# Optimization experiments

Measured on AMD Instinct MI355X. Metric: run time of the kernel, lower is better.

The kernel has to match this reference:

```python
import jax, jax.numpy as jnp
import numpy as np

ALPHA, BETA, GAMMA = 1.0, 0.01, 0.1
COS_EPS = 1e-8  # torch F.cosine_similarity eps


def setup_inputs() -> dict:
    key = jax.random.key(0)
    k1, k2, k3, k4 = jax.random.split(key, 4)
    B, C = 4096, 1000
    N, D = 8192, 256
    return {
        "pred": jax.random.normal(k1, (B, C), dtype=jnp.float32),
        "target": jax.random.randint(k2, (B,), 0, C, dtype=jnp.int64),
        "adj_matrix": jax.random.uniform(k3, (N, N), dtype=jnp.float32),
        "node_embeddings": jax.random.normal(k4, (N, D), dtype=jnp.float32),
    }


def reference(pred, target, adj_matrix, node_embeddings):
    # L_task: mean cross-entropy over logits
    logp = jax.nn.log_softmax(pred, axis=-1)                      # [B, C]
    l_task = -jnp.mean(jnp.take_along_axis(logp, target[:, None], axis=1))

    # L_sparse: mean |adj|
    l_sparse = jnp.mean(jnp.abs(adj_matrix))

    # L_semantic: cosine similarity via normalize + matmul (avoids NxNxD intermediate)
    norms = jnp.linalg.norm(node_embeddings, axis=1)              # [N]
    dots = node_embeddings @ node_embeddings.T                    # [N, N]
    sim = dots / jnp.maximum(norms[:, None] * norms[None, :], COS_EPS)
    l_semantic = jnp.mean(adj_matrix * (1.0 - sim))

    return ALPHA * l_task + BETA * l_sparse + GAMMA * l_semantic
```

## Files before the change

### kernel.cpp

```cpp
#include <hip/hip_runtime.h>
#include <hip/hip_bf16.h>
#include <stdint.h>
#include <stddef.h>

#define N_NODES 8192
#define DIM     256
#define BATCH   4096
#define CLASSES 1000
#define ALPHA_C 1.0f
#define BETA_C  0.01f
#define GAMMA_C 0.1f

#define KSPLIT  16
#define KRANGE  (N_NODES / KSPLIT)
#define NCHUNK  (KRANGE / 64)
#define BM      64

typedef __bf16 bf16_t;
typedef __bf16 bf16x8 __attribute__((ext_vector_type(8)));
typedef float  f32x4  __attribute__((ext_vector_type(4)));
typedef float  f32x16 __attribute__((ext_vector_type(16)));

__device__ __forceinline__ void async16(const void* g, void* l) {
  __builtin_amdgcn_global_load_lds(
      (const __attribute__((address_space(1))) uint32_t*)g,
      (__attribute__((address_space(3))) uint32_t*)l, 16, 0, 0);
}

__global__ __launch_bounds__(256) void prep_norm(
    const float* __restrict__ emb, bf16_t* __restrict__ U) {
  const int row = blockIdx.x;
  const int t = threadIdx.x;
  const float v = emb[(size_t)row * DIM + t];
  float sq = v * v;
  for (int off = 32; off; off >>= 1) sq += __shfl_down(sq, off);
  __shared__ float red[4];
  if ((t & 63) == 0) red[t >> 6] = sq;
  __syncthreads();
  const float total = red[0] + red[1] + red[2] + red[3];
  U[(size_t)row * DIM + t] = (bf16_t)(v * rsqrtf(total));
}

#define TP 68

__global__ __launch_bounds__(256) void prep_transpose(
    const bf16_t* __restrict__ U, bf16_t* __restrict__ V) {
  __shared__ bf16_t tile[64 * TP];
  const int k0 = blockIdx.x * 64;
  const int d0 = blockIdx.y * 64;
  const int t = threadIdx.x;
  const int r = t >> 3;
  const int c8 = t & 7;

  *(bf16x8*)&tile[r * TP + c8 * 8] =
      *(const bf16x8*)&U[(size_t)(k0 + r) * DIM + d0 + c8 * 8];
  *(bf16x8*)&tile[(r + 32) * TP + c8 * 8] =
      *(const bf16x8*)&U[(size_t)(k0 + r + 32) * DIM + d0 + c8 * 8];
  __syncthreads();

  bf16x8 o0, o1;
#pragma unroll
  for (int j = 0; j < 8; ++j) {
    o0[j] = tile[(c8 * 8 + j) * TP + r];
    o1[j] = tile[(c8 * 8 + j) * TP + r + 32];
  }
  *(bf16x8*)&V[(size_t)(d0 + r) * N_NODES + k0 + c8 * 8] = o0;
  *(bf16x8*)&V[(size_t)(d0 + r + 32) * N_NODES + k0 + c8 * 8] = o1;
}

__global__ __launch_bounds__(256) void ce_kernel(
    const float* __restrict__ pred, const int* __restrict__ target,
    float* __restrict__ out) {
  const int row = blockIdx.x;
  const int t = threadIdx.x;
  const float* p = pred + (size_t)row * CLASSES;

  float v[4];
  for (int k = 0; k < 4; ++k) {
    const int c = t + k * 256;
    v[k] = (c < CLASSES) ? p[c] : -INFINITY;
  }

  float m = fmaxf(fmaxf(v[0], v[1]), fmaxf(v[2], v[3]));
  for (int off = 32; off; off >>= 1) m = fmaxf(m, __shfl_down(m, off));

  __shared__ float red[8];
  const int wave = t >> 6, lane = t & 63;
  if (lane == 0) red[wave] = m;
  __syncthreads();
  if (t == 0) red[4] = fmaxf(fmaxf(red[0], red[1]), fmaxf(red[2], red[3]));
  __syncthreads();
  const float mx = red[4];

  float s = 0.f;
  for (int k = 0; k < 4; ++k) s += __expf(v[k] - mx);
  for (int off = 32; off; off >>= 1) s += __shfl_down(s, off);
  if (lane == 0) red[wave] = s;
  __syncthreads();
  if (t == 0) {
    float ssum = red[0] + red[1] + red[2] + red[3];
    float lse = mx + __logf(ssum);
    float loss = lse - p[target[row]];
    atomicAdd(out, loss * (ALPHA_C / (float)BATCH));
  }
}

__global__ __launch_bounds__(256) void gemm_kernel(
    const float* __restrict__ adj, const bf16_t* __restrict__ U,
    const bf16_t* __restrict__ V, float* __restrict__ out) {
  __shared__ __align__(16) bf16_t As[BM * 64];
  __shared__ __align__(16) bf16_t Bs[DIM * 64];

  const int i0 = blockIdx.x * BM;
  const int kbase = blockIdx.y * KRANGE;
  const int t = threadIdx.x;
  const int w = t >> 6, lane = t & 63;
  const int m = lane & 31, h = lane >> 5;

  const int ar = t >> 3;
  const int ac = t & 7;
  const int srow = lane >> 3;
  const int sch = (lane & 7) ^ srow;

  f32x16 acc[2][2] = {};
  float sa = 0.f, sabs = 0.f;

  float4 pf[4];
  {
    const float* a0p = adj + (size_t)(i0 + ar) * N_NODES + kbase + ac * 8;
    const float* a1p = adj + (size_t)(i0 + ar + 32) * N_NODES + kbase + ac * 8;
    pf[0] = *(const float4*)a0p;
    pf[1] = *(const float4*)(a0p + 4);
    pf[2] = *(const float4*)a1p;
    pf[3] = *(const float4*)(a1p + 4);
  }

  for (int kc = 0; kc < NCHUNK; ++kc) {
    const int k0 = kbase + kc * 64;

#pragma unroll
    for (int s = 0; s < 8; ++s) {
      const int dbase = w * 64 + s * 8;
      async16(V + (size_t)(dbase + srow) * N_NODES + k0 + sch * 8,
              &Bs[dbase * 64]);
    }

    {
      bf16x8 c0, c1;
      c0[0] = (bf16_t)pf[0].x; c0[1] = (bf16_t)pf[0].y;
      c0[2] = (bf16_t)pf[0].z; c0[3] = (bf16_t)pf[0].w;
      c0[4] = (bf16_t)pf[1].x; c0[5] = (bf16_t)pf[1].y;
      c0[6] = (bf16_t)pf[1].z; c0[7] = (bf16_t)pf[1].w;
      c1[0] = (bf16_t)pf[2].x; c1[1] = (bf16_t)pf[2].y;
      c1[2] = (bf16_t)pf[2].z; c1[3] = (bf16_t)pf[2].w;
      c1[4] = (bf16_t)pf[3].x; c1[5] = (bf16_t)pf[3].y;
      c1[6] = (bf16_t)pf[3].z; c1[7] = (bf16_t)pf[3].w;
#pragma unroll
      for (int q = 0; q < 4; ++q) {
        sa += pf[q].x + pf[q].y + pf[q].z + pf[q].w;
        sabs += fabsf(pf[q].x) + fabsf(pf[q].y) +
                fabsf(pf[q].z) + fabsf(pf[q].w);
      }
      const int p = (ac ^ (ar & 7)) * 8;
      *(bf16x8*)&As[ar * 64 + p] = c0;
      *(bf16x8*)&As[(ar + 32) * 64 + p] = c1;
    }
    __syncthreads();

    if (kc + 1 < NCHUNK) {
      const int kn = k0 + 64;
      const float* a0p = adj + (size_t)(i0 + ar) * N_NODES + kn + ac * 8;
      const float* a1p = adj + (size_t)(i0 + ar + 32) * N_NODES + kn + ac * 8;
      pf[0] = *(const float4*)a0p;
      pf[1] = *(const float4*)(a0p + 4);
      pf[2] = *(const float4*)a1p;
      pf[3] = *(const float4*)(a1p + 4);
    }

#pragma unroll
    for (int kk = 0; kk < 4; ++kk) {
      const int p = ((kk * 2 + h) ^ (m & 7)) * 8;
      bf16x8 a0 = *(const bf16x8*)&As[m * 64 + p];
      bf16x8 a1 = *(const bf16x8*)&As[(m + 32) * 64 + p];
      bf16x8 b0 = *(const bf16x8*)&Bs[(w * 64 + m) * 64 + p];
      bf16x8 b1 = *(const bf16x8*)&Bs[(w * 64 + 32 + m) * 64 + p];
      acc[0][0] =
          __builtin_amdgcn_mfma_f32_32x32x16_bf16(a0, b0, acc[0][0], 0, 0, 0);
      acc[0][1] =
          __builtin_amdgcn_mfma_f32_32x32x16_bf16(a0, b1, acc[0][1], 0, 0, 0);
      acc[1][0] =
          __builtin_amdgcn_mfma_f32_32x32x16_bf16(a1, b0, acc[1][0], 0, 0, 0);
      acc[1][1] =
          __builtin_amdgcn_mfma_f32_32x32x16_bf16(a1, b1, acc[1][1], 0, 0, 0);
    }
    __syncthreads();
  }

  float simdot = 0.f;
#pragma unroll
  for (int mi = 0; mi < 2; ++mi) {
#pragma unroll
    for (int nd = 0; nd < 2; ++nd) {
      const int ib = i0 + mi * 32 + 4 * h;
      const int d = w * 64 + nd * 32 + m;
      const bf16_t* up = U + (size_t)ib * DIM + d;
#pragma unroll
      for (int rg = 0; rg < 16; ++rg) {
        const int row = (rg & 3) + 8 * (rg >> 2);
        simdot += (float)up[(size_t)row * DIM] * acc[mi][nd][rg];
      }
    }
  }

  float local = BETA_C * sabs + GAMMA_C * (sa - simdot);
  for (int off = 32; off; off >>= 1) local += __shfl_down(local, off);
  float* redf = (float*)As;
  if (lane == 0) redf[w] = local;
  __syncthreads();
  if (t == 0) {
    const float inv = 1.f / ((float)N_NODES * (float)N_NODES);
    atomicAdd(out, (redf[0] + redf[1] + redf[2] + redf[3]) * inv);
  }
}

extern "C" void kernel_launch(void* const* d_in, const int* in_sizes, int n_in,
                              void* d_out, int out_size, void* d_ws,
                              size_t ws_size, hipStream_t stream) {
  const float* pred   = (const float*)d_in[0];
  const int*   target = (const int*)d_in[1];
  const float* adj    = (const float*)d_in[2];
  const float* emb    = (const float*)d_in[3];
  float* out = (float*)d_out;

  bf16_t* U = (bf16_t*)d_ws;
  bf16_t* V = (bf16_t*)((char*)d_ws + (size_t)N_NODES * DIM * 2);

  hipMemsetAsync(d_out, 0, sizeof(float), stream);
  ce_kernel<<<BATCH, 256, 0, stream>>>(pred, target, out);
  prep_norm<<<N_NODES, 256, 0, stream>>>(emb, U);
  prep_transpose<<<dim3(N_NODES / 64, DIM / 64), 256, 0, stream>>>(U, V);
  gemm_kernel<<<dim3(N_NODES / BM, KSPLIT), 256, 0, stream>>>(adj, U, V, out);
}
```

Measured before the change: 487.0 us.

## Preload the block's whole adjacency slice into registers and stage wide A tiles

The GEMM kernel now issues every adjacency load for its 64x512 slice at kernel start: 32 float4 per thread, arranged as 16 rows per wave. These fill two 256-wide super-chunks. Each super-chunk is converted to bf16 into a larger XOR-swizzled LDS A tile, and the per-wave B tile is streamed in 64-wide steps over it. This aims to raise memory-level parallelism on the dominant fp32 adjacency stream and to cut the block-wide barriers per 64-column step. The cost is heavy register use (128 VGPRs of prefetch plus the accumulators) and 64KB of LDS per block under a 2-blocks-per-CU bound, which may limit occupancy or cause spills.

```diff
diff --git a/kernel.cpp b/kernel.cpp
--- a/kernel.cpp
+++ b/kernel.cpp
@@ -13,10 +13,14 @@
 
 #define KSPLIT  16
 #define KRANGE  (N_NODES / KSPLIT)
-#define NCHUNK  (KRANGE / 64)
+#define SUPER   256
+#define NSUPER  (KRANGE / SUPER)
+#define BK      64
+#define NBK     (SUPER / BK)
 #define BM      64
 
 typedef __bf16 bf16_t;
+typedef __bf16 bf16x4 __attribute__((ext_vector_type(4)));
 typedef __bf16 bf16x8 __attribute__((ext_vector_type(8)));
 typedef float  f32x4  __attribute__((ext_vector_type(4)));
 typedef float  f32x16 __attribute__((ext_vector_type(16)));
@@ -105,95 +109,81 @@
   }
 }
 
-__global__ __launch_bounds__(256) void gemm_kernel(
+__global__ __launch_bounds__(256, 2) void gemm_kernel(
     const float* __restrict__ adj, const bf16_t* __restrict__ U,
     const bf16_t* __restrict__ V, float* __restrict__ out) {
-  __shared__ __align__(16) bf16_t As[BM * 64];
-  __shared__ __align__(16) bf16_t Bs[DIM * 64];
+  __shared__ __align__(16) bf16_t As[BM * SUPER];
+  __shared__ __align__(16) bf16_t Bs[DIM * BK];
+  __shared__ float red[4];
 
   const int i0 = blockIdx.x * BM;
   const int kbase = blockIdx.y * KRANGE;
   const int t = threadIdx.x;
   const int w = t >> 6, lane = t & 63;
   const int m = lane & 31, h = lane >> 5;
-
-  const int ar = t >> 3;
-  const int ac = t & 7;
   const int srow = lane >> 3;
   const int sch = (lane & 7) ^ srow;
 
+  const float* arow =
+      adj + (size_t)(i0 + w * 16) * N_NODES + kbase + lane * 4;
+  float4 pf0[16], pf1[16];
+#pragma unroll
+  for (int j = 0; j < 16; ++j)
+    pf0[j] = *(const float4*)(arow + (size_t)j * N_NODES);
+#pragma unroll
+  for (int j = 0; j < 16; ++j)
+    pf1[j] = *(const float4*)(arow + (size_t)j * N_NODES + SUPER);
+
   f32x16 acc[2][2] = {};
   float sa = 0.f, sabs = 0.f;
 
-  float4 pf[4];
-  {
-    const float* a0p = adj + (size_t)(i0 + ar) * N_NODES + kbase + ac * 8;
-    const float* a1p = adj + (size_t)(i0 + ar + 32) * N_NODES + kbase + ac * 8;
-    pf[0] = *(const float4*)a0p;
-    pf[1] = *(const float4*)(a0p + 4);
-    pf[2] = *(const float4*)a1p;
-    pf[3] = *(const float4*)(a1p + 4);
-  }
-
-  for (int kc = 0; kc < NCHUNK; ++kc) {
-    const int k0 = kbase + kc * 64;
-
-#pragma unroll
-    for (int s = 0; s < 8; ++s) {
-      const int dbase = w * 64 + s * 8;
-      async16(V + (size_t)(dbase + srow) * N_NODES + k0 + sch * 8,
-              &Bs[dbase * 64]);
+#pragma unroll
+  for (int s = 0; s < NSUPER; ++s) {
+    __syncthreads();
+
+#pragma unroll
+    for (int j = 0; j < 16; ++j) {
+      const float4 v = s ? pf1[j] : pf0[j];
+      sa += v.x + v.y + v.z + v.w;
+      sabs += fabsf(v.x) + fabsf(v.y) + fabsf(v.z) + fabsf(v.w);
+      const int r = w * 16 + j;
+      bf16x4 c;
+      c[0] = (bf16_t)v.x; c[1] = (bf16_t)v.y;
+      c[2] = (bf16_t)v.z; c[3] = (bf16_t)v.w;
+      const int pos = (((lane >> 1) ^ (r & 31)) & 31) * 8 + (lane & 1) * 4;
+      *(bf16x4*)&As[r * SUPER + pos] = c;
     }
 
-    {
-      bf16x8 c0, c1;
-      c0[0] = (bf16_t)pf[0].x; c0[1] = (bf16_t)pf[0].y;
-      c0[2] = (bf16_t)pf[0].z; c0[3] = (bf16_t)pf[0].w;
-      c0[4] = (bf16_t)pf[1].x; c0[5] = (bf16_t)pf[1].y;
-      c0[6] = (bf16_t)pf[1].z; c0[7] = (bf16_t)pf[1].w;
-      c1[0] = (bf16_t)pf[2].x; c1[1] = (bf16_t)pf[2].y;
-      c1[2] = (bf16_t)pf[2].z; c1[3] = (bf16_t)pf[2].w;
-      c1[4] = (bf16_t)pf[3].x; c1[5] = (bf16_t)pf[3].y;
-      c1[6] = (bf16_t)pf[3].z; c1[7] = (bf16_t)pf[3].w;
-#pragma unroll
-      for (int q = 0; q < 4; ++q) {
-        sa += pf[q].x + pf[q].y + pf[q].z + pf[q].w;
-        sabs += fabsf(pf[q].x) + fabsf(pf[q].y) +
-                fabsf(pf[q].z) + fabsf(pf[q].w);
+#pragma unroll
+    for (int bk = 0; bk < NBK; ++bk) {
+      const int k0 = kbase + s * SUPER + bk * BK;
+#pragma unroll
+      for (int q = 0; q < 8; ++q) {
+        const int dbase = w * 64 + q * 8;
+        async16(V + (size_t)(dbase + srow) * N_NODES + k0 + sch * 8,
+                &Bs[dbase * 64]);
       }
-      const int p = (ac ^ (ar & 7)) * 8;
-      *(bf16x8*)&As[ar * 64 + p] = c0;
-      *(bf16x8*)&As[(ar + 32) * 64 + p] = c1;
+      __syncthreads();
+
+#pragma unroll
+      for (int kk = 0; kk < 4; ++kk) {
+        const int qa = bk * 8 + kk * 2 + h;
+        const int pa = ((qa ^ m) & 31) * 8;
+        bf16x8 a0 = *(const bf16x8*)&As[m * SUPER + pa];
+        bf16x8 a1 = *(const bf16x8*)&As[(m + 32) * SUPER + pa];
+        const int pb = ((kk * 2 + h) ^ (m & 7)) * 8;
+        bf16x8 b0 = *(const bf16x8*)&Bs[(w * 64 + m) * 64 + pb];
+        bf16x8 b1 = *(const bf16x8*)&Bs[(w * 64 + 32 + m) * 64 + pb];
+        acc[0][0] = __builtin_amdgcn_mfma_f32_32x32x16_bf16(a0, b0, acc[0][0],
+                                                            0, 0, 0);
+        acc[0][1] = __builtin_amdgcn_mfma_f32_32x32x16_bf16(a0, b1, acc[0][1],
+                                                            0, 0, 0);
+        acc[1][0] = __builtin_amdgcn_mfma_f32_32x32x16_bf16(a1, b0, acc[1][0],
+                                                            0, 0, 0);
+        acc[1][1] = __builtin_amdgcn_mfma_f32_32x32x16_bf16(a1, b1, acc[1][1],
+                                                            0, 0, 0);
+      }
     }
-    __syncthreads();
-
-    if (kc + 1 < NCHUNK) {
-      const int kn = k0 + 64;
-      const float* a0p = adj + (size_t)(i0 + ar) * N_NODES + kn + ac * 8;
-      const float* a1p = adj + (size_t)(i0 + ar + 32) * N_NODES + kn + ac * 8;
-      pf[0] = *(const float4*)a0p;
-      pf[1] = *(const float4*)(a0p + 4);
-      pf[2] = *(const float4*)a1p;
-      pf[3] = *(const float4*)(a1p + 4);
-    }
-
-#pragma unroll
-    for (int kk = 0; kk < 4; ++kk) {
-      const int p = ((kk * 2 + h) ^ (m & 7)) * 8;
-      bf16x8 a0 = *(const bf16x8*)&As[m * 64 + p];
-      bf16x8 a1 = *(const bf16x8*)&As[(m + 32) * 64 + p];
-      bf16x8 b0 = *(const bf16x8*)&Bs[(w * 64 + m) * 64 + p];
-      bf16x8 b1 = *(const bf16x8*)&Bs[(w * 64 + 32 + m) * 64 + p];
-      acc[0][0] =
-          __builtin_amdgcn_mfma_f32_32x32x16_bf16(a0, b0, acc[0][0], 0, 0, 0);
-      acc[0][1] =
-          __builtin_amdgcn_mfma_f32_32x32x16_bf16(a0, b1, acc[0][1], 0, 0, 0);
-      acc[1][0] =
-          __builtin_amdgcn_mfma_f32_32x32x16_bf16(a1, b0, acc[1][0], 0, 0, 0);
-      acc[1][1] =
-          __builtin_amdgcn_mfma_f32_32x32x16_bf16(a1, b1, acc[1][1], 0, 0, 0);
-    }
-    __syncthreads();
   }
 
   float simdot = 0.f;
@@ -214,12 +204,11 @@
 
   float local = BETA_C * sabs + GAMMA_C * (sa - simdot);
   for (int off = 32; off; off >>= 1) local += __shfl_down(local, off);
-  float* redf = (float*)As;
-  if (lane == 0) redf[w] = local;
+  if (lane == 0) red[w] = local;
   __syncthreads();
   if (t == 0) {
     const float inv = 1.f / ((float)N_NODES * (float)N_NODES);
-    atomicAdd(out, (redf[0] + redf[1] + redf[2] + redf[3]) * inv);
+    atomicAdd(out, (red[0] + red[1] + red[2] + red[3]) * inv);
   }
 }
 
```

Result: slower. 506.8 us (+4.1%).
